# Kernel tuning notes

Hardware: AMD Instinct MI355X
Metric: run time of the kernel (lower is better)

Reference implementation:

```python
import jax, jax.numpy as jnp
import numpy as np

B, S, H, NH = 4, 2048, 768, 12
HD = H // NH

def _ln(x, g, b, eps=1e-5):
    m = jnp.mean(x, -1, keepdims=True)
    v = jnp.mean((x - m) ** 2, -1, keepdims=True)
    return (x - m) * jax.lax.rsqrt(v + eps) * g + b

def setup_inputs() -> dict:
    key = jax.random.key(0)
    ks = jax.random.split(key, 16)
    s = 0.02
    return {
        "x": jax.random.normal(ks[0], (B, S, H), jnp.float32),
        "prev_state": jax.random.normal(ks[1], (B, S, H), jnp.float32),
        "mask": jax.random.randint(ks[2], (B,), 0, 2).astype(bool),
        # depthwise conv1d (groups=H, k=3): torch weight [H, 1, 3] == OIH
        "conv_dw_w": jax.random.normal(ks[3], (H, 1, 3), jnp.float32) * s,
        "conv_dw_b": jnp.zeros((H,), jnp.float32),
        # pointwise conv1d (k=1) stored as [out, in]
        "conv_pw_w": jax.random.normal(ks[4], (H, H), jnp.float32) * s,
        "conv_pw_b": jnp.zeros((H,), jnp.float32),
        "cn_g": jnp.ones((H,), jnp.float32), "cn_b": jnp.zeros((H,), jnp.float32),
        "Wq": jax.random.normal(ks[5], (H, H), jnp.float32) * s, "bq": jnp.zeros((H,), jnp.float32),
        "Wk": jax.random.normal(ks[6], (H, H), jnp.float32) * s, "bk": jnp.zeros((H,), jnp.float32),
        "Wv": jax.random.normal(ks[7], (H, H), jnp.float32) * s, "bv": jnp.zeros((H,), jnp.float32),
        "Wo": jax.random.normal(ks[8], (H, H), jnp.float32) * s, "bo": jnp.zeros((H,), jnp.float32),
        "pn_g": jnp.ones((H,), jnp.float32), "pn_b": jnp.zeros((H,), jnp.float32),
        "Wpost": jax.random.normal(ks[9], (H, H), jnp.float32) * s, "bpost": jnp.zeros((H,), jnp.float32),
        "Wg": jax.random.normal(ks[10], (1, 2 * H), jnp.float32) * s, "bg": jnp.zeros((1,), jnp.float32),
    }

def reference(x, prev_state, mask, conv_dw_w, conv_dw_b, conv_pw_w, conv_pw_b,
              cn_g, cn_b, Wq, bq, Wk, bk, Wv, bv, Wo, bo,
              pn_g, pn_b, Wpost, bpost, Wg, bg):
    # ---- bridge: depthwise conv (k=3) -> pointwise conv (k=1) -> GELU -> LN ----
    mem_t = prev_state.transpose(0, 2, 1)  # [B, H, S]
    dw = jax.lax.conv_general_dilated(
        mem_t, conv_dw_w, window_strides=(1,), padding=[(1, 1)],
        feature_group_count=H, dimension_numbers=("NCH", "OIH", "NCH")) + conv_dw_b[None, :, None]
    pw = jnp.einsum("bhs,oh->bos", dw, conv_pw_w) + conv_pw_b[None, :, None]
    bridged = jax.nn.gelu(pw, approximate=False).transpose(0, 2, 1)  # [B, S, H]
    bridged = _ln(bridged, cn_g, cn_b)
    # ---- cross attention: q from x, k/v from bridged memory (nope, non-causal) ----
    q = (jnp.einsum("bsh,oh->bso", x, Wq) + bq).reshape(B, S, NH, HD)
    k = (jnp.einsum("bsh,oh->bso", bridged, Wk) + bk).reshape(B, S, NH, HD)
    v = (jnp.einsum("bsh,oh->bso", bridged, Wv) + bv).reshape(B, S, NH, HD)
    scores = jnp.einsum("bqnd,bknd->bnqk", q, k) / np.float32(np.sqrt(HD))
    attn = jax.nn.softmax(scores, axis=-1)
    ao = jnp.einsum("bnqk,bknd->bqnd", attn, v).reshape(B, S, H)
    ao = jnp.einsum("bsh,oh->bso", ao, Wo) + bo
    # ---- post-attn norm, linear, gate, scatter-add back under mask ----
    inj = _ln(ao, pn_g, pn_b)
    inj = jnp.einsum("bsh,oh->bso", inj, Wpost) + bpost
    gate = jax.nn.sigmoid(jnp.einsum("bsh,oh->bso", jnp.concatenate([x, bridged], -1), Wg) + bg)
    gated = gate * jnp.tanh(inj)
    mf = mask.astype(x.dtype)[:, None, None]  # batch-row select == masked scatter-add
    out = x + mf * gated
    # masked MSE aux loss (only over selected rows, as in the original)
    denom = jnp.maximum(mask.sum(), 1).astype(x.dtype) * np.float32(S * H)
    aux = jnp.sum(mf * (bridged - x) ** 2) / denom
    return out, aux
```

## Files before the change

kernel.cpp:

```cpp
#include <hip/hip_runtime.h>
#include <math.h>

#define B_ 4
#define S_ 2048
#define H_ 768
#define NH_ 12
#define HD_ 64
#define BSH (B_ * S_ * H_)
#define NROWS (B_ * S_)
#define WSZ (H_ * H_)

typedef __attribute__((ext_vector_type(8))) short bf16x8;
typedef __attribute__((ext_vector_type(4))) short s16x4;
typedef __attribute__((ext_vector_type(4))) float f32x4;
typedef __attribute__((ext_vector_type(2))) unsigned u32x2;
typedef __attribute__((ext_vector_type(4))) unsigned u32x4;

__device__ __forceinline__ short f2bf(float f) {
  union { float f; unsigned u; } x; x.f = f;
  unsigned r = x.u + 0x7FFF + ((x.u >> 16) & 1);
  return (short)(r >> 16);
}
__device__ __forceinline__ float bf2f(short s) {
  union { unsigned u; float f; } x;
  x.u = ((unsigned)(unsigned short)s) << 16;
  return x.f;
}
__device__ __forceinline__ unsigned bfpack(float lo, float hi) {
  union { float f; unsigned u; } a, b; a.f = lo; b.f = hi;
  return __builtin_amdgcn_perm(b.u, a.u, 0x07060302);
}

__device__ __forceinline__ float fexp2(float x) {
#if __has_builtin(__builtin_amdgcn_exp2f)
  return __builtin_amdgcn_exp2f(x);
#else
  float r;
  asm("v_exp_f32 %0, %1" : "=v"(r) : "v"(x));
  return r;
#endif
}

__device__ __forceinline__ void plswap32(unsigned& a, unsigned& b) {
#if __has_builtin(__builtin_amdgcn_permlane32_swap)
  u32x2 r = __builtin_amdgcn_permlane32_swap(a, b, false, false);
  a = r.x; b = r.y;
#else
  asm volatile("v_permlane32_swap_b32 %0, %1" : "+v"(a), "+v"(b));
#endif
}
__device__ __forceinline__ void plswap16(unsigned& a, unsigned& b) {
#if __has_builtin(__builtin_amdgcn_permlane16_swap)
  u32x2 r = __builtin_amdgcn_permlane16_swap(a, b, false, false);
  a = r.x; b = r.y;
#else
  asm volatile("v_permlane16_swap_b32 %0, %1" : "+v"(a), "+v"(b));
#endif
}

typedef __attribute__((address_space(1))) const unsigned int g_u32;
typedef __attribute__((address_space(3))) unsigned int l_u32;
__device__ __forceinline__ void gload16(const void* g, void* l) {
  __builtin_amdgcn_global_load_lds((g_u32*)g, (l_u32*)l, 16, 0, 0);
}

__global__ __launch_bounds__(256) void cvt_x_k(const float* __restrict__ src,
                                               short* __restrict__ dst) {
  int i = (blockIdx.x * 256 + threadIdx.x) * 4;
  float4 v = *(const float4*)(src + i);
  s16x4 o = {f2bf(v.x), f2bf(v.y), f2bf(v.z), f2bf(v.w)};
  *(s16x4*)(dst + i) = o;
}

__global__ __launch_bounds__(256) void cvt6_k(const float* w0, const float* w1,
                                              const float* w2, const float* w3,
                                              const float* w4, const float* w5,
                                              short* __restrict__ dst) {
  int i = (blockIdx.x * 256 + threadIdx.x) * 4;
  int m = i / WSZ;
  int off = i - m * WSZ;
  const float* s = m == 0 ? w0 : m == 1 ? w1 : m == 2 ? w2 : m == 3 ? w3 : m == 4 ? w4 : w5;
  float sc = (m == 1) ? 0.1803368802f : 1.0f;
  float4 v = *(const float4*)(s + off);
  s16x4 o = {f2bf(v.x * sc), f2bf(v.y * sc), f2bf(v.z * sc), f2bf(v.w * sc)};
  *(s16x4*)(dst + i) = o;
}

__global__ __launch_bounds__(192) void dwconv_k(const float* __restrict__ prev,
                                                const float* __restrict__ w3,
                                                const float* __restrict__ bias,
                                                short* __restrict__ out) {
  int row = blockIdx.x;
  int s = row & (S_ - 1);
  int h = threadIdx.x * 4;
  size_t base = (size_t)row * H_ + h;
  float4 c = *(const float4*)(prev + base);
  float4 wa = *(const float4*)(w3 + h * 3);
  float4 wb = *(const float4*)(w3 + h * 3 + 4);
  float4 wc = *(const float4*)(w3 + h * 3 + 8);
  float4 bi = *(const float4*)(bias + h);
  float4 acc;
  acc.x = bi.x + c.x * wa.y;
  acc.y = bi.y + c.y * wb.x;
  acc.z = bi.z + c.z * wb.w;
  acc.w = bi.w + c.w * wc.z;
  if (s > 0) {
    float4 l = *(const float4*)(prev + base - H_);
    acc.x += l.x * wa.x; acc.y += l.y * wa.w; acc.z += l.z * wb.z; acc.w += l.w * wc.y;
  }
  if (s < S_ - 1) {
    float4 r = *(const float4*)(prev + base + H_);
    acc.x += r.x * wa.z; acc.y += r.y * wb.y; acc.z += r.z * wc.x; acc.w += r.w * wc.w;
  }
  s16x4 o = {f2bf(acc.x), f2bf(acc.y), f2bf(acc.z), f2bf(acc.w)};
  *(s16x4*)(out + base) = o;
}

struct GemmJob {
  const short* A; const short* W; const float* bias; short* C; int act; int tout;
  float bscale;
};

__global__ __launch_bounds__(256) void gemm_bf2(GemmJob j0, GemmJob j1, GemmJob j2) {
  int d = blockIdx.x;
  int z = d / 384, r5 = d - z * 384;
  GemmJob j = z == 0 ? j0 : (z == 1 ? j1 : j2);
  int xcd = r5 & 7, s5 = r5 >> 3;
  int nx = s5 % 6, ny = xcd + 8 * (s5 / 6);
  __shared__ short As[2][128 * 64];
  __shared__ short Ws[2][128 * 64];
  int tid = threadIdx.x, lane = tid & 63, w = tid >> 6;
  int wr = w >> 1, wc = w & 1, lm = lane & 15, lq = lane >> 4;
  int lm7 = lm & 7;
  int rb8 = (lq ^ lm7) << 3, rb8x = rb8 ^ 32;
  int m0 = ny * 128, n0 = nx * 128;
  int srow = lane >> 3;
  int jl = ((lane & 7) ^ srow) * 8;
  const short* gA = j.A + (size_t)(m0 + w * 32 + srow) * H_ + jl;
  const short* gW = j.W + (size_t)(n0 + w * 32 + srow) * H_ + jl;
  int lbase = w * 2048;

  f32x4 acc[4][4];
#pragma unroll
  for (int i = 0; i < 4; ++i)
#pragma unroll
    for (int jj = 0; jj < 4; ++jj) acc[i][jj] = (f32x4){0.f, 0.f, 0.f, 0.f};

#pragma unroll
  for (int c = 0; c < 4; ++c) {
    gload16(gA + (size_t)(c * 8) * H_, &As[0][lbase + c * 512]);
    gload16(gW + (size_t)(c * 8) * H_, &Ws[0][lbase + c * 512]);
  }

  for (int kt = 0, pb = 0; kt < H_; kt += 64, pb ^= 1) {
    __syncthreads();
    if (kt + 64 < H_) {
#pragma unroll
      for (int c = 0; c < 4; ++c) {
        gload16(gA + kt + 64 + (size_t)(c * 8) * H_, &As[pb ^ 1][lbase + c * 512]);
        gload16(gW + kt + 64 + (size_t)(c * 8) * H_, &Ws[pb ^ 1][lbase + c * 512]);
      }
    }
    const short* Aw = &As[pb][0];
    const short* Ww = &Ws[pb][0];
#pragma unroll
    for (int kk = 0; kk < 2; ++kk) {
      int ro = kk ? rb8x : rb8;
      bf16x8 af[4], wf[4];
#pragma unroll
      for (int i = 0; i < 4; ++i)
        af[i] = *(const bf16x8*)&Aw[(wr * 64 + i * 16 + lm) * 64 + ro];
#pragma unroll
      for (int jj = 0; jj < 4; ++jj)
        wf[jj] = *(const bf16x8*)&Ww[(wc * 64 + jj * 16 + lm) * 64 + ro];
#pragma unroll
      for (int i = 0; i < 4; ++i)
#pragma unroll
        for (int jj = 0; jj < 4; ++jj)
          acc[i][jj] = __builtin_amdgcn_mfma_f32_16x16x32_bf16(af[i], wf[jj], acc[i][jj], 0, 0, 0);
    }
  }

  if (!j.tout) {
#pragma unroll
    for (int jj = 0; jj < 4; ++jj) {
      int col = n0 + wc * 64 + jj * 16 + lm;
      float bn = j.bias[col] * j.bscale;
#pragma unroll
      for (int i = 0; i < 4; ++i) {
        int mrow = m0 + wr * 64 + i * 16 + lq * 4;
#pragma unroll
        for (int r = 0; r < 4; ++r) {
          float cv = acc[i][jj][r] + bn;
          if (j.act) cv = 0.5f * cv * (1.0f + erff(cv * 0.70710678118f));
          j.C[(size_t)(mrow + r) * H_ + col] = f2bf(cv);
        }
      }
    }
  } else {
    int b = m0 >> 11;
    int sb = (m0 & (S_ - 1)) + wr * 64;
#pragma unroll
    for (int jj = 0; jj < 4; ++jj) {
      int col = n0 + wc * 64 + jj * 16 + lm;
      float bn = j.bias[col] * j.bscale;
      short* cp = j.C + ((size_t)(b * H_ + col)) * S_;
#pragma unroll
      for (int i = 0; i < 4; ++i) {
        int s = sb + i * 16 + lq * 4;
        s16x4 pk = {f2bf(acc[i][jj][0] + bn), f2bf(acc[i][jj][1] + bn),
                    f2bf(acc[i][jj][2] + bn), f2bf(acc[i][jj][3] + bn)};
        *(s16x4*)(cp + s) = pk;
      }
    }
  }
}

__global__ __launch_bounds__(256) void gemm_n64(const short* __restrict__ A,
                                                const short* __restrict__ W,
                                                const float* __restrict__ bias,
                                                short* __restrict__ C, int act) {
  int d = blockIdx.x;
  int xcd = d & 7, s5 = d >> 3;
  int nx = s5 % 12, ny = xcd + 8 * (s5 / 12);
  __shared__ short As[2][128 * 64];
  __shared__ short Ws[2][64 * 64];
  int tid = threadIdx.x, lane = tid & 63, w = tid >> 6;
  int wm = w >> 1, wn = w & 1, lm = lane & 15, lq = lane >> 4;
  int lm7 = lm & 7;
  int rb8 = (lq ^ lm7) << 3, rb8x = rb8 ^ 32;
  int m0 = ny * 128, n0 = nx * 64;
  int srow = lane >> 3;
  int jl = ((lane & 7) ^ srow) * 8;
  const short* gA = A + (size_t)(m0 + w * 32 + srow) * H_ + jl;
  const short* gW = W + (size_t)(n0 + w * 16 + srow) * H_ + jl;
  int lbaseA = w * 2048;
  int lbaseW = w * 1024;

  f32x4 acc[4][2];
#pragma unroll
  for (int i = 0; i < 4; ++i)
#pragma unroll
    for (int jj = 0; jj < 2; ++jj) acc[i][jj] = (f32x4){0.f, 0.f, 0.f, 0.f};

#pragma unroll
  for (int c = 0; c < 4; ++c)
    gload16(gA + (size_t)(c * 8) * H_, &As[0][lbaseA + c * 512]);
#pragma unroll
  for (int c = 0; c < 2; ++c)
    gload16(gW + (size_t)(c * 8) * H_, &Ws[0][lbaseW + c * 512]);

  for (int kt = 0, pb = 0; kt < H_; kt += 64, pb ^= 1) {
    __syncthreads();
    if (kt + 64 < H_) {
#pragma unroll
      for (int c = 0; c < 4; ++c)
        gload16(gA + kt + 64 + (size_t)(c * 8) * H_, &As[pb ^ 1][lbaseA + c * 512]);
#pragma unroll
      for (int c = 0; c < 2; ++c)
        gload16(gW + kt + 64 + (size_t)(c * 8) * H_, &Ws[pb ^ 1][lbaseW + c * 512]);
    }
    const short* Aw = &As[pb][0];
    const short* Ww = &Ws[pb][0];
#pragma unroll
    for (int kk = 0; kk < 2; ++kk) {
      int ro = kk ? rb8x : rb8;
      bf16x8 af[4], wf[2];
#pragma unroll
      for (int i = 0; i < 4; ++i)
        af[i] = *(const bf16x8*)&Aw[(wm * 64 + i * 16 + lm) * 64 + ro];
#pragma unroll
      for (int jj = 0; jj < 2; ++jj)
        wf[jj] = *(const bf16x8*)&Ww[(wn * 32 + jj * 16 + lm) * 64 + ro];
#pragma unroll
      for (int i = 0; i < 4; ++i)
#pragma unroll
        for (int jj = 0; jj < 2; ++jj)
          acc[i][jj] = __builtin_amdgcn_mfma_f32_16x16x32_bf16(af[i], wf[jj], acc[i][jj], 0, 0, 0);
    }
  }

#pragma unroll
  for (int jj = 0; jj < 2; ++jj) {
    int col = n0 + wn * 32 + jj * 16 + lm;
    float bn = bias[col];
#pragma unroll
    for (int i = 0; i < 4; ++i) {
      int mrow = m0 + wm * 64 + i * 16 + lq * 4;
#pragma unroll
      for (int r = 0; r < 4; ++r) {
        float cv = acc[i][jj][r] + bn;
        if (act) cv = 0.5f * cv * (1.0f + erff(cv * 0.70710678118f));
        C[(size_t)(mrow + r) * H_ + col] = f2bf(cv);
      }
    }
  }
}

__global__ __launch_bounds__(256) void ln_bf(const short* __restrict__ X,
                                             short* __restrict__ Y,
                                             const float* __restrict__ g,
                                             const float* __restrict__ bb) {
  int row = blockIdx.x;
  size_t base = (size_t)row * H_;
  int h0 = threadIdx.x, h1 = h0 + 256, h2 = h0 + 512;
  float x0 = bf2f(X[base + h0]), x1 = bf2f(X[base + h1]), x2 = bf2f(X[base + h2]);
  float s = x0 + x1 + x2;
  float s2 = x0 * x0 + x1 * x1 + x2 * x2;
  for (int off = 32; off > 0; off >>= 1) {
    s += __shfl_down(s, off);
    s2 += __shfl_down(s2, off);
  }
  __shared__ float sa[4], sq[4], st[2];
  int wid = threadIdx.x >> 6, lane = threadIdx.x & 63;
  if (lane == 0) { sa[wid] = s; sq[wid] = s2; }
  __syncthreads();
  if (threadIdx.x == 0) {
    float ts = sa[0] + sa[1] + sa[2] + sa[3];
    float ts2 = sq[0] + sq[1] + sq[2] + sq[3];
    float mean = ts * (1.0f / H_);
    float var = ts2 * (1.0f / H_) - mean * mean;
    st[0] = mean;
    st[1] = rsqrtf(var + 1e-5f);
  }
  __syncthreads();
  float mean = st[0], rstd = st[1];
  Y[base + h0] = f2bf((x0 - mean) * rstd * g[h0] + bb[h0]);
  Y[base + h1] = f2bf((x1 - mean) * rstd * g[h1] + bb[h1]);
  Y[base + h2] = f2bf((x2 - mean) * rstd * g[h2] + bb[h2]);
}

__global__ __launch_bounds__(256) void attn8_k(const short* __restrict__ qb,
                                               const short* __restrict__ kb,
                                               const short* __restrict__ vtb,
                                               short* __restrict__ aob) {
  __shared__ short Ks[2][64 * 64];
  __shared__ short Vt[2][64 * 64];
  int tid = threadIdx.x, lane = tid & 63, w = tid >> 6;
  int lm = lane & 15, lq = lane >> 4;
  int lm7 = lm & 7;
  int dd = blockIdx.x;
  int xcd = dd & 7, slot = dd >> 3;
  int g = xcd + 8 * (slot >> 4);
  int qx = slot & 15;
  int b = g / NH_, n = g - b * NH_;
  int q0 = qx * 128;
  int hoff = n * HD_;

  int rb8 = (lq ^ lm7) << 3;
  int rb8x = rb8 ^ 32;

  bf16x8 qf[2][2];
#pragma unroll
  for (int qg = 0; qg < 2; ++qg) {
    const short* qrow = qb + ((size_t)(b * S_ + q0 + w * 32 + qg * 16 + lm)) * H_ + hoff;
    qf[qg][0] = *(const bf16x8*)(qrow + lq * 8);
    qf[qg][1] = *(const bf16x8*)(qrow + 32 + lq * 8);
  }

  bf16x8 onef = {0x3F80, 0x3F80, 0x3F80, 0x3F80, 0x3F80, 0x3F80, 0x3F80, 0x3F80};
  f32x4 ls[2];
  ls[0] = (f32x4){0.f, 0.f, 0.f, 0.f};
  ls[1] = (f32x4){0.f, 0.f, 0.f, 0.f};

  f32x4 o[4][2];
#pragma unroll
  for (int i = 0; i < 4; ++i)
#pragma unroll
    for (int qg = 0; qg < 2; ++qg) o[i][qg] = (f32x4){0.f, 0.f, 0.f, 0.f};

  int jl = ((lane & 7) ^ (lane >> 3)) * 8;
  int rr = w * 16 + (lane >> 3);
  const short* kgl = kb + ((size_t)(b * S_ + rr)) * H_ + hoff + jl;
  const short* vgl = vtb + ((size_t)(b * H_ + hoff + rr)) * S_ + jl;
  int lbase = w * 1024;

#pragma unroll
  for (int c = 0; c < 2; ++c) {
    gload16(kgl + (size_t)(c * 8) * H_, &Ks[0][lbase + c * 512]);
    gload16(vgl + (size_t)(c * 8) * S_, &Vt[0][lbase + c * 512]);
  }

  for (int kt = 0, pb = 0; kt < S_; kt += 64, pb ^= 1) {
    __syncthreads();
    if (kt + 64 < S_) {
#pragma unroll
      for (int c = 0; c < 2; ++c) {
        gload16(kgl + (size_t)(kt + 64 + c * 8) * H_, &Ks[pb ^ 1][lbase + c * 512]);
        gload16(vgl + (size_t)(c * 8) * S_ + (kt + 64), &Vt[pb ^ 1][lbase + c * 512]);
      }
    }
    const short* Kw = &Ks[pb][0];
    const short* Vw = &Vt[pb][0];

    f32x4 st[4][2];
    __builtin_amdgcn_s_setprio(1);
#pragma unroll
    for (int ni = 0; ni < 4; ++ni) {
      int krow = (ni * 16 + lm) * 64;
      bf16x8 ka0 = *(const bf16x8*)&Kw[krow + rb8];
      bf16x8 ka1 = *(const bf16x8*)&Kw[krow + rb8x];
#pragma unroll
      for (int qg = 0; qg < 2; ++qg) {
        f32x4 z = (f32x4){0.f, 0.f, 0.f, 0.f};
        z = __builtin_amdgcn_mfma_f32_16x16x32_bf16(ka0, qf[qg][0], z, 0, 0, 0);
        st[ni][qg] = __builtin_amdgcn_mfma_f32_16x16x32_bf16(ka1, qf[qg][1], z, 0, 0, 0);
      }
    }
    __builtin_amdgcn_s_setprio(0);

    bf16x8 pf[2][2];
#pragma unroll
    for (int qg = 0; qg < 2; ++qg) {
      unsigned pw0, pw1, pw2, pw3, pw4, pw5, pw6, pw7;
      {
        float p0 = fexp2(st[0][qg][0]), p1 = fexp2(st[0][qg][1]);
        float p2 = fexp2(st[0][qg][2]), p3 = fexp2(st[0][qg][3]);
        pw0 = bfpack(p0, p1); pw1 = bfpack(p2, p3);
      }
      {
        float p0 = fexp2(st[1][qg][0]), p1 = fexp2(st[1][qg][1]);
        float p2 = fexp2(st[1][qg][2]), p3 = fexp2(st[1][qg][3]);
        pw2 = bfpack(p0, p1); pw3 = bfpack(p2, p3);
      }
      {
        float p0 = fexp2(st[2][qg][0]), p1 = fexp2(st[2][qg][1]);
        float p2 = fexp2(st[2][qg][2]), p3 = fexp2(st[2][qg][3]);
        pw4 = bfpack(p0, p1); pw5 = bfpack(p2, p3);
      }
      {
        float p0 = fexp2(st[3][qg][0]), p1 = fexp2(st[3][qg][1]);
        float p2 = fexp2(st[3][qg][2]), p3 = fexp2(st[3][qg][3]);
        pw6 = bfpack(p0, p1); pw7 = bfpack(p2, p3);
      }
      plswap32(pw0, pw2); plswap16(pw0, pw2);
      plswap32(pw1, pw3); plswap16(pw1, pw3);
      plswap32(pw4, pw6); plswap16(pw4, pw6);
      plswap32(pw5, pw7); plswap16(pw5, pw7);
      union { u32x4 u; bf16x8 v; } c0u, c1u;
      c0u.u = (u32x4){pw0, pw1, pw2, pw3};
      c1u.u = (u32x4){pw4, pw5, pw6, pw7};
      pf[qg][0] = c0u.v;
      pf[qg][1] = c1u.v;
    }

    __builtin_amdgcn_s_setprio(1);
#pragma unroll
    for (int qg = 0; qg < 2; ++qg) {
      ls[qg] = __builtin_amdgcn_mfma_f32_16x16x32_bf16(onef, pf[qg][0], ls[qg], 0, 0, 0);
      ls[qg] = __builtin_amdgcn_mfma_f32_16x16x32_bf16(onef, pf[qg][1], ls[qg], 0, 0, 0);
    }
#pragma unroll
    for (int nd = 0; nd < 4; ++nd) {
      int vrow = (nd * 16 + lm) * 64;
      bf16x8 va0 = *(const bf16x8*)&Vw[vrow + rb8];
      bf16x8 va1 = *(const bf16x8*)&Vw[vrow + rb8x];
#pragma unroll
      for (int qg = 0; qg < 2; ++qg) {
        o[nd][qg] = __builtin_amdgcn_mfma_f32_16x16x32_bf16(va0, pf[qg][0], o[nd][qg], 0, 0, 0);
        o[nd][qg] = __builtin_amdgcn_mfma_f32_16x16x32_bf16(va1, pf[qg][1], o[nd][qg], 0, 0, 0);
      }
    }
    __builtin_amdgcn_s_setprio(0);
  }

#pragma unroll
  for (int qg = 0; qg < 2; ++qg) {
    float inv = 1.0f / ls[qg][0];
    short* orow = aob + ((size_t)(b * S_ + q0 + w * 32 + qg * 16 + lm)) * H_ + hoff;
#pragma unroll
    for (int nd = 0; nd < 4; ++nd) {
      s16x4 pk = {f2bf(o[nd][qg][0] * inv), f2bf(o[nd][qg][1] * inv),
                  f2bf(o[nd][qg][2] * inv), f2bf(o[nd][qg][3] * inv)};
      *(s16x4*)(orow + nd * 16 + lq * 4) = pk;
    }
  }
}

__global__ __launch_bounds__(192) void gate_out_k(const float* __restrict__ x,
                                                  const short* __restrict__ br,
                                                  const short* __restrict__ inj,
                                                  const int* __restrict__ mask,
                                                  const float* __restrict__ Wg,
                                                  const float* __restrict__ bg,
                                                  float* __restrict__ out,
                                                  float* __restrict__ paux) {
  int row = blockIdx.x;
  int b = row >> 11;
  size_t base = (size_t)row * H_;
  int h = threadIdx.x * 4;
  float4 xv = *(const float4*)(x + base + h);
  s16x4 brv = *(const s16x4*)(br + base + h);
  s16x4 inv = *(const s16x4*)(inj + base + h);
  float4 wg0 = *(const float4*)(Wg + h);
  float4 wg1 = *(const float4*)(Wg + H_ + h);
  float b0 = bf2f(brv.x), b1 = bf2f(brv.y), b2 = bf2f(brv.z), b3 = bf2f(brv.w);
  float dot = xv.x * wg0.x + xv.y * wg0.y + xv.z * wg0.z + xv.w * wg0.w
            + b0 * wg1.x + b1 * wg1.y + b2 * wg1.z + b3 * wg1.w;
  float d0 = b0 - xv.x, d1 = b1 - xv.y, d2 = b2 - xv.z, d3 = b3 - xv.w;
  float aux = d0 * d0 + d1 * d1 + d2 * d2 + d3 * d3;
  for (int off = 32; off > 0; off >>= 1) {
    dot += __shfl_down(dot, off);
    aux += __shfl_down(aux, off);
  }
  __shared__ float sd[3], sx[3], gsh[2];
  int wid = threadIdx.x >> 6, lane = threadIdx.x & 63;
  if (lane == 0) { sd[wid] = dot; sx[wid] = aux; }
  __syncthreads();
  if (threadIdx.x == 0) {
    float td = sd[0] + sd[1] + sd[2];
    float ta = sx[0] + sx[1] + sx[2];
    gsh[0] = 1.0f / (1.0f + expf(-(td + bg[0])));
    gsh[1] = ta;
  }
  __syncthreads();
  float mf = (mask[b] != 0) ? 1.0f : 0.0f;
  float gm = gsh[0] * mf;
  float v0 = bf2f(inv.x), v1 = bf2f(inv.y), v2 = bf2f(inv.z), v3 = bf2f(inv.w);
  float e0 = __expf(2.f * v0), e1 = __expf(2.f * v1), e2 = __expf(2.f * v2), e3 = __expf(2.f * v3);
  float4 ov;
  ov.x = xv.x + gm * ((e0 - 1.f) / (e0 + 1.f));
  ov.y = xv.y + gm * ((e1 - 1.f) / (e1 + 1.f));
  ov.z = xv.z + gm * ((e2 - 1.f) / (e2 + 1.f));
  ov.w = xv.w + gm * ((e3 - 1.f) / (e3 + 1.f));
  *(float4*)(out + base + h) = ov;
  if (threadIdx.x == 0) paux[row] = mf * gsh[1];
}

__global__ __launch_bounds__(256) void aux_reduce_k(const float* __restrict__ paux,
                                                    const int* __restrict__ mask,
                                                    float* __restrict__ outp) {
  float s = 0.f;
  for (int i = threadIdx.x; i < NROWS; i += 256) s += paux[i];
  for (int off = 32; off > 0; off >>= 1) s += __shfl_down(s, off);
  __shared__ float sw[4];
  int wid = threadIdx.x >> 6, lane = threadIdx.x & 63;
  if (lane == 0) sw[wid] = s;
  __syncthreads();
  if (threadIdx.x == 0) {
    float t = sw[0] + sw[1] + sw[2] + sw[3];
    int nm = (mask[0] != 0) + (mask[1] != 0) + (mask[2] != 0) + (mask[3] != 0);
    if (nm < 1) nm = 1;
    outp[0] = t / ((float)nm * (float)(S_ * H_));
  }
}

extern "C" void kernel_launch(void* const* d_in, const int* in_sizes, int n_in,
                              void* d_out, int out_size, void* d_ws, size_t ws_size,
                              hipStream_t stream) {
  const float* x     = (const float*)d_in[0];
  const float* prev  = (const float*)d_in[1];
  const int*   mask  = (const int*)d_in[2];
  const float* dw_w  = (const float*)d_in[3];
  const float* dw_b  = (const float*)d_in[4];
  const float* pw_w  = (const float*)d_in[5];
  const float* pw_b  = (const float*)d_in[6];
  const float* cn_g  = (const float*)d_in[7];
  const float* cn_b  = (const float*)d_in[8];
  const float* Wq    = (const float*)d_in[9];
  const float* bq    = (const float*)d_in[10];
  const float* Wk    = (const float*)d_in[11];
  const float* bk    = (const float*)d_in[12];
  const float* Wv    = (const float*)d_in[13];
  const float* bv    = (const float*)d_in[14];
  const float* Wo    = (const float*)d_in[15];
  const float* bo    = (const float*)d_in[16];
  const float* pn_g  = (const float*)d_in[17];
  const float* pn_b  = (const float*)d_in[18];
  const float* Wpost = (const float*)d_in[19];
  const float* bpost = (const float*)d_in[20];
  const float* Wg    = (const float*)d_in[21];
  const float* bg    = (const float*)d_in[22];
  float* out = (float*)d_out;

  short* B0 = (short*)d_ws;
  short* B1 = B0 + BSH;
  short* B2 = B1 + BSH;
  short* B3 = B2 + BSH;
  short* B4 = B3 + BSH;
  short* B5 = B4 + BSH;
  short* WW = B5 + BSH;
  float* paux = (float*)(WW + 6 * WSZ);

  const float C1 = 0.1803368802f;

  GemmJob jq = {B0, WW + WSZ,     bq, B1, 0, 0, C1};
  GemmJob jk = {B3, WW + 2 * WSZ, bk, B4, 0, 0, 1.0f};
  GemmJob jv = {B3, WW + 3 * WSZ, bv, B5, 0, 1, 1.0f};

  cvt6_k<<<6 * WSZ / 1024, 256, 0, stream>>>(pw_w, Wq, Wk, Wv, Wo, Wpost, WW);
  cvt_x_k<<<BSH / 1024, 256, 0, stream>>>(x, B0);
  dwconv_k<<<NROWS, 192, 0, stream>>>(prev, dw_w, dw_b, B1);
  gemm_n64<<<768, 256, 0, stream>>>(B1, WW, pw_b, B2, 1);
  ln_bf<<<NROWS, 256, 0, stream>>>(B2, B3, cn_g, cn_b);
  gemm_bf2<<<1152, 256, 0, stream>>>(jq, jk, jv);
  attn8_k<<<768, 256, 0, stream>>>(B1, B4, B5, B2);
  gemm_n64<<<768, 256, 0, stream>>>(B2, WW + 4 * WSZ, bo, B4, 0);
  ln_bf<<<NROWS, 256, 0, stream>>>(B4, B4, pn_g, pn_b);
  gemm_n64<<<768, 256, 0, stream>>>(B4, WW + 5 * WSZ, bpost, B5, 0);
  gate_out_k<<<NROWS, 192, 0, stream>>>(x, B3, B5, mask, Wg, bg, out, paux);
  aux_reduce_k<<<1, 256, 0, stream>>>(paux, mask, out + BSH);
}
```

Before: 369.4 us.

## Triple-buffer A tiles with explicit vmcnt waits and add occupancy launch bounds

Reworks the gemm_bf2 main loop so A tiles are prefetched two stages ahead in a three-slot LDS ring while W tiles stay double-buffered. Partial s_waitcnt vmcnt replaces the full __syncthreads wait, letting loads for later stages stay in flight across the barrier. It also adds min-blocks-per-CU hints to gemm_bf2, gemm_n64 and attn8_k to push for higher occupancy. The cost is more LDS per gemm_bf2 block and tighter register limits that could cause spills.

```diff
diff --git a/kernel.cpp b/kernel.cpp
--- a/kernel.cpp
+++ b/kernel.cpp
@@ -121,17 +121,17 @@
   float bscale;
 };
 
-__global__ __launch_bounds__(256) void gemm_bf2(GemmJob j0, GemmJob j1, GemmJob j2) {
+__global__ __launch_bounds__(256, 2) void gemm_bf2(GemmJob j0, GemmJob j1, GemmJob j2) {
   int d = blockIdx.x;
   int z = d / 384, r5 = d - z * 384;
   GemmJob j = z == 0 ? j0 : (z == 1 ? j1 : j2);
   int xcd = r5 & 7, s5 = r5 >> 3;
   int nx = s5 % 6, ny = xcd + 8 * (s5 / 6);
-  __shared__ short As[2][128 * 64];
+  __shared__ short As[3][128 * 64];
   __shared__ short Ws[2][128 * 64];
   int tid = threadIdx.x, lane = tid & 63, w = tid >> 6;
   int wr = w >> 1, wc = w & 1, lm = lane & 15, lq = lane >> 4;
-  int lm7 = lm & 7;
+  int lm7 = lm & 15 & 7;
   int rb8 = (lq ^ lm7) << 3, rb8x = rb8 ^ 32;
   int m0 = ny * 128, n0 = nx * 128;
   int srow = lane >> 3;
@@ -147,22 +147,36 @@
     for (int jj = 0; jj < 4; ++jj) acc[i][jj] = (f32x4){0.f, 0.f, 0.f, 0.f};
 
 #pragma unroll
-  for (int c = 0; c < 4; ++c) {
+  for (int c = 0; c < 4; ++c)
     gload16(gA + (size_t)(c * 8) * H_, &As[0][lbase + c * 512]);
+#pragma unroll
+  for (int c = 0; c < 4; ++c)
     gload16(gW + (size_t)(c * 8) * H_, &Ws[0][lbase + c * 512]);
-  }
-
-  for (int kt = 0, pb = 0; kt < H_; kt += 64, pb ^= 1) {
-    __syncthreads();
-    if (kt + 64 < H_) {
-#pragma unroll
-      for (int c = 0; c < 4; ++c) {
-        gload16(gA + kt + 64 + (size_t)(c * 8) * H_, &As[pb ^ 1][lbase + c * 512]);
-        gload16(gW + kt + 64 + (size_t)(c * 8) * H_, &Ws[pb ^ 1][lbase + c * 512]);
-      }
-    }
-    const short* Aw = &As[pb][0];
-    const short* Ww = &Ws[pb][0];
+#pragma unroll
+  for (int c = 0; c < 4; ++c)
+    gload16(gA + 64 + (size_t)(c * 8) * H_, &As[1][lbase + c * 512]);
+
+  const int NST = H_ / 64;
+  for (int t = 0; t < NST; ++t) {
+    if (t < NST - 1) asm volatile("s_waitcnt vmcnt(4)" ::: "memory");
+    else             asm volatile("s_waitcnt vmcnt(0)" ::: "memory");
+    __builtin_amdgcn_s_barrier();
+    __builtin_amdgcn_sched_barrier(0);
+    if (t + 1 < NST) {
+      int kt1 = (t + 1) * 64;
+#pragma unroll
+      for (int c = 0; c < 4; ++c)
+        gload16(gW + kt1 + (size_t)(c * 8) * H_, &Ws[(t + 1) & 1][lbase + c * 512]);
+    }
+    if (t + 2 < NST) {
+      int kt2 = (t + 2) * 64;
+      int a2 = (t + 2) % 3;
+#pragma unroll
+      for (int c = 0; c < 4; ++c)
+        gload16(gA + kt2 + (size_t)(c * 8) * H_, &As[a2][lbase + c * 512]);
+    }
+    const short* Aw = &As[t % 3][0];
+    const short* Ww = &Ws[t & 1][0];
 #pragma unroll
     for (int kk = 0; kk < 2; ++kk) {
       int ro = kk ? rb8x : rb8;
@@ -216,10 +230,10 @@
   }
 }
 
-__global__ __launch_bounds__(256) void gemm_n64(const short* __restrict__ A,
-                                                const short* __restrict__ W,
-                                                const float* __restrict__ bias,
-                                                short* __restrict__ C, int act) {
+__global__ __launch_bounds__(256, 3) void gemm_n64(const short* __restrict__ A,
+                                                   const short* __restrict__ W,
+                                                   const float* __restrict__ bias,
+                                                   short* __restrict__ C, int act) {
   int d = blockIdx.x;
   int xcd = d & 7, s5 = d >> 3;
   int nx = s5 % 12, ny = xcd + 8 * (s5 / 12);
@@ -330,10 +344,10 @@
   Y[base + h2] = f2bf((x2 - mean) * rstd * g[h2] + bb[h2]);
 }
 
-__global__ __launch_bounds__(256) void attn8_k(const short* __restrict__ qb,
-                                               const short* __restrict__ kb,
-                                               const short* __restrict__ vtb,
-                                               short* __restrict__ aob) {
+__global__ __launch_bounds__(256, 3) void attn8_k(const short* __restrict__ qb,
+                                                  const short* __restrict__ kb,
+                                                  const short* __restrict__ vtb,
+                                                  short* __restrict__ aob) {
   __shared__ short Ks[2][64 * 64];
   __shared__ short Vt[2][64 * 64];
   int tid = threadIdx.x, lane = tid & 63, w = tid >> 6;
```

After: 358.9 us. -2.8%, faster.
